# Kernel tuning notes

Hardware: AMD Instinct MI355X
Metric: run time of the kernel (lower is better)

## Reference

```python
import jax, jax.numpy as jnp
import numpy as np

B, S, D_IN, D_OUT = 4, 4096, 1024, 64

def setup_inputs() -> dict:
    key = jax.random.key(0)
    ks = jax.random.split(key, 7)
    return {
        "x":  jax.random.normal(ks[0], (B, S, D_IN), dtype=jnp.float32),
        "Wq": jax.random.normal(ks[1], (D_IN, D_OUT), dtype=jnp.float32) * 0.02,
        "bq": jax.random.normal(ks[2], (D_OUT,), dtype=jnp.float32) * 0.02,
        "Wk": jax.random.normal(ks[3], (D_IN, D_OUT), dtype=jnp.float32) * 0.02,
        "bk": jax.random.normal(ks[4], (D_OUT,), dtype=jnp.float32) * 0.02,
        "Wv": jax.random.normal(ks[5], (D_IN, D_OUT), dtype=jnp.float32) * 0.02,
        "bv": jax.random.normal(ks[6], (D_OUT,), dtype=jnp.float32) * 0.02,
    }

def reference(x, Wq, bq, Wk, bk, Wv, bv):
    # x: [B, S, d_in]
    seq = x.shape[1]
    q = x @ Wq + bq            # [B, S, d_out]
    k = x @ Wk + bk
    v = x @ Wv + bv
    scores = jnp.einsum("bqd,bkd->bqk", q, k)          # [B, S, S]
    causal = jnp.triu(jnp.ones((seq, seq), dtype=bool), k=1)
    scores = jnp.where(causal[None, :, :], -jnp.inf, scores)
    # NOTE: original code scales by sqrt(token_len), not sqrt(d_out) (d_k = keys.shape[1])
    scale = jnp.sqrt(jnp.asarray(seq, dtype=scores.dtype))
    attn = jax.nn.softmax(scores / scale, axis=-1)      # [B, S, S]
    # dropout in the original is applied but its result is discarded -> no-op
    return jnp.einsum("bqk,bkd->bqd", attn, v)          # [B, S, d_out]
```

## Files before the change

kernel.cpp:

```cpp
#include <hip/hip_runtime.h>
#include <math.h>

#define B 4
#define S 4096
#define DIN 1024
#define DOUT 64
#define BS (B * S)

typedef __bf16 bf16;
typedef __bf16 bf16x4 __attribute__((ext_vector_type(4)));
typedef __bf16 bf16x8 __attribute__((ext_vector_type(8)));
typedef float f32x4 __attribute__((ext_vector_type(4)));

#define QSCALE 0.022542110013890053f

#define QS_OFF 0
#define KF_OFF (2u * 1024 * 1024)
#define VF_OFF (4u * 1024 * 1024)
#define WP_OFF (6u * 1024 * 1024)
#define OP_OFF (7u * 1024 * 1024)
#define LP_OFF (23u * 1024 * 1024)

__global__ __launch_bounds__(256) void wpack_kernel(
    const float* __restrict__ Wq, const float* __restrict__ Wk,
    const float* __restrict__ Wv, bf16* __restrict__ wp) {
  const int t = blockIdx.x * 256 + threadIdx.x;
  const int m = t >> 16;
  const int r = t & 65535;
  const int k = r >> 6;
  const int n64 = r & 63;
  const float* W = (m == 0) ? Wq : (m == 1) ? Wk : Wv;
  const float v = W[r];
  const int n = m * 64 + n64;
  const int nt = n >> 4;
  const int lane = ((k >> 3) & 3) * 16 + (n & 15);
  const int idx = ((nt * 32 + (k >> 5)) * 64 + lane) * 8 + (k & 7);
  wp[idx] = (bf16)v;
}

__global__ __launch_bounds__(256) void qkv_mfma_kernel(
    const float* __restrict__ x, const float* __restrict__ bq,
    const float* __restrict__ bk, const float* __restrict__ bv,
    const bf16* __restrict__ wp, bf16* __restrict__ Qs,
    bf16* __restrict__ KF, bf16* __restrict__ VF) {
  __shared__ __align__(16) bf16 xt[32][520];

  const int tid = threadIdx.x;
  const int wid = tid >> 6;
  const int lane = tid & 63;
  const int l15 = lane & 15;
  const int quad = lane >> 4;
  const int blk = blockIdx.x;

  const bf16x8* wp8 = (const bf16x8*)wp;

  f32x4 acc[3][2];
#pragma unroll
  for (int j = 0; j < 3; ++j)
#pragma unroll
    for (int st = 0; st < 2; ++st) acc[j][st] = (f32x4)(0.f);

  for (int ph = 0; ph < 2; ++ph) {
    if (ph) __syncthreads();
    {
      float4 v[16];
#pragma unroll
      for (int i = 0; i < 16; ++i) {
        const int ch = i * 256 + tid;
        const int row = ch >> 7;
        const int col4 = ch & 127;
        v[i] = *(const float4*)(x + (size_t)(blk * 32 + row) * DIN + ph * 512 +
                                col4 * 4);
      }
#pragma unroll
      for (int i = 0; i < 16; ++i) {
        const int ch = i * 256 + tid;
        const int row = ch >> 7;
        const int col4 = ch & 127;
        bf16x4 c;
        c[0] = (bf16)v[i].x; c[1] = (bf16)v[i].y;
        c[2] = (bf16)v[i].z; c[3] = (bf16)v[i].w;
        *(bf16x4*)&xt[row][col4 * 4] = c;
      }
    }
    __syncthreads();

#pragma unroll 4
    for (int kc = 0; kc < 16; ++kc) {
      bf16x8 bfr[3];
#pragma unroll
      for (int j = 0; j < 3; ++j)
        bfr[j] = wp8[((wid * 3 + j) * 32 + ph * 16 + kc) * 64 + lane];
      const bf16x8 a0 = *(const bf16x8*)&xt[l15][quad * 8 + kc * 32];
      const bf16x8 a1 = *(const bf16x8*)&xt[16 + l15][quad * 8 + kc * 32];
#pragma unroll
      for (int j = 0; j < 3; ++j) {
        acc[j][0] = __builtin_amdgcn_mfma_f32_16x16x32_bf16(a0, bfr[j], acc[j][0], 0, 0, 0);
        acc[j][1] = __builtin_amdgcn_mfma_f32_16x16x32_bf16(a1, bfr[j], acc[j][1], 0, 0, 0);
      }
    }
  }

#pragma unroll
  for (int j = 0; j < 3; ++j) {
    const int nt = wid * 3 + j;
    const int sel = nt >> 2;
    const int c = (nt & 3) * 16 + l15;
    const float bias = ((sel == 0) ? bq : (sel == 1) ? bk : bv)[c];
#pragma unroll
    for (int st = 0; st < 2; ++st) {
      const int row0 = blk * 32 + st * 16 + quad * 4;
      if (sel == 0) {
#pragma unroll
        for (int r = 0; r < 4; ++r)
          Qs[(size_t)(row0 + r) * DOUT + c] =
              (bf16)((acc[j][st][r] + bias) * QSCALE);
      } else if (sel == 1) {
        const size_t kb =
            ((size_t)(((row0 >> 6) * 4 + ((row0 >> 4) & 3)) * 2 + (c >> 5)) * 64 +
             ((c >> 3) & 3) * 16 + quad * 4) * 8 + (c & 7);
#pragma unroll
        for (int r = 0; r < 4; ++r)
          KF[kb + r * 8] = (bf16)(acc[j][st][r] + bias);
      } else {
        const size_t vb =
            ((size_t)(((row0 >> 6) * 2 + ((row0 >> 5) & 1)) * 4 + (c >> 4)) * 64 +
             (c & 15) + 16 * ((row0 >> 3) & 3)) * 8 + (row0 & 7);
        bf16x4 vv;
#pragma unroll
        for (int r = 0; r < 4; ++r) vv[r] = (bf16)(acc[j][st][r] + bias);
        *(bf16x4*)(VF + vb) = vv;
      }
    }
  }
}

__global__ __launch_bounds__(256) void attn_mfma_kernel(
    const bf16* __restrict__ Qs, const bf16* __restrict__ KFp,
    const bf16* __restrict__ VFp, bf16* __restrict__ Oh,
    float* __restrict__ lh) {
  __shared__ __align__(16) bf16 pw[4][32][72];

  const int tid = threadIdx.x;
  const int wid = tid >> 6;
  const int lane = tid & 63;
  const int l15 = lane & 15;
  const int quad = lane >> 4;
  const int b = blockIdx.x & 3;
  const int half = (blockIdx.x >> 2) & 1;
  const int s32 = 127 - (blockIdx.x >> 3);
  const int ntiles = (s32 >> 1) + 1;
  const int e = half * 4 + wid;
  const int t0 = (e * ntiles) >> 3;
  const int t1 = ((e + 1) * ntiles) >> 3;

  const bf16x8* KF8 = (const bf16x8*)KFp;
  const bf16x8* VF8 = (const bf16x8*)VFp;
  const int tb0 = b * 64;

  const bf16* Qb = Qs + ((size_t)b * S + s32 * 32) * DOUT;
  bf16x8 qf[2][2];
#pragma unroll
  for (int st = 0; st < 2; ++st)
#pragma unroll
    for (int k = 0; k < 2; ++k)
      qf[st][k] =
          *(const bf16x8*)(Qb + (st * 16 + l15) * DOUT + k * 32 + quad * 8);

  f32x4 o[2][4];
#pragma unroll
  for (int st = 0; st < 2; ++st)
#pragma unroll
    for (int i = 0; i < 4; ++i) o[st][i] = (f32x4)(0.f);
  f32x4 lsum[2] = {(f32x4)(0.f), (f32x4)(0.f)};

  for (int t = t0; t < t1; ++t) {
    const int tb = tb0 + t;
    bf16x8 kf[8], vf[8];
#pragma unroll
    for (int nt = 0; nt < 4; ++nt)
#pragma unroll
      for (int c = 0; c < 2; ++c)
        kf[nt * 2 + c] = KF8[(size_t)((tb * 4 + nt) * 2 + c) * 64 + lane];
#pragma unroll
    for (int c = 0; c < 2; ++c)
#pragma unroll
      for (int ntd = 0; ntd < 4; ++ntd)
        vf[c * 4 + ntd] = VF8[(size_t)((tb * 2 + c) * 4 + ntd) * 64 + lane];

    f32x4 s[2][4];
#pragma unroll
    for (int st = 0; st < 2; ++st)
#pragma unroll
      for (int nt = 0; nt < 4; ++nt) {
        s[st][nt] = __builtin_amdgcn_mfma_f32_16x16x32_bf16(
            qf[st][0], kf[nt * 2 + 0], (f32x4)(0.f), 0, 0, 0);
        s[st][nt] = __builtin_amdgcn_mfma_f32_16x16x32_bf16(
            qf[st][1], kf[nt * 2 + 1], s[st][nt], 0, 0, 0);
      }

    if (t == ntiles - 1) {
#pragma unroll
      for (int st = 0; st < 2; ++st)
#pragma unroll
        for (int nt = 0; nt < 4; ++nt) {
          const int key = t * 64 + nt * 16 + l15;
#pragma unroll
          for (int r = 0; r < 4; ++r) {
            const int qrow = s32 * 32 + st * 16 + quad * 4 + r;
            const float p = (key <= qrow) ? exp2f(fminf(s[st][nt][r], 44.f)) : 0.f;
            lsum[st][r] += p;
            pw[wid][st * 16 + quad * 4 + r][nt * 16 + l15] = (bf16)p;
          }
        }
    } else {
#pragma unroll
      for (int st = 0; st < 2; ++st)
#pragma unroll
        for (int nt = 0; nt < 4; ++nt)
#pragma unroll
          for (int r = 0; r < 4; ++r) {
            const float p = exp2f(fminf(s[st][nt][r], 44.f));
            lsum[st][r] += p;
            pw[wid][st * 16 + quad * 4 + r][nt * 16 + l15] = (bf16)p;
          }
    }

#pragma unroll
    for (int st = 0; st < 2; ++st) {
      const bf16x8 pf0 = *(const bf16x8*)&pw[wid][st * 16 + l15][quad * 8];
      const bf16x8 pf1 = *(const bf16x8*)&pw[wid][st * 16 + l15][32 + quad * 8];
#pragma unroll
      for (int ntd = 0; ntd < 4; ++ntd) {
        o[st][ntd] = __builtin_amdgcn_mfma_f32_16x16x32_bf16(
            pf0, vf[0 * 4 + ntd], o[st][ntd], 0, 0, 0);
        o[st][ntd] = __builtin_amdgcn_mfma_f32_16x16x32_bf16(
            pf1, vf[1 * 4 + ntd], o[st][ntd], 0, 0, 0);
      }
    }
  }

#pragma unroll
  for (int m = 1; m < 16; m <<= 1)
#pragma unroll
    for (int st = 0; st < 2; ++st)
#pragma unroll
      for (int r = 0; r < 4; ++r) lsum[st][r] += __shfl_xor(lsum[st][r], m, 64);

  const int slot = (b * 128 + s32) * 8 + e;
  if (l15 == 0) {
#pragma unroll
    for (int st = 0; st < 2; ++st)
#pragma unroll
      for (int r = 0; r < 4; ++r)
        lh[slot * 32 + st * 16 + quad * 4 + r] = lsum[st][r];
  }
#pragma unroll
  for (int st = 0; st < 2; ++st)
#pragma unroll
    for (int ntd = 0; ntd < 4; ++ntd)
#pragma unroll
      for (int r = 0; r < 4; ++r)
        Oh[(size_t)slot * 2048 + (st * 16 + quad * 4 + r) * 64 + ntd * 16 + l15] =
            (bf16)o[st][ntd][r];
}

__global__ __launch_bounds__(256) void combine_kernel(
    const bf16* __restrict__ Oh, const float* __restrict__ lh,
    float* __restrict__ out) {
  const int gid = blockIdx.x * 256 + threadIdx.x;
  const int token = gid >> 4;
  const int d4 = (gid & 15) * 4;
  const int b = token >> 12;
  const int s = token & 4095;
  const int s32 = s >> 5;
  const int qq = s & 31;
  const int slot0 = (b * 128 + s32) * 8;
  f32x4 acc = (f32x4)(0.f);
  float l = 0.f;
#pragma unroll
  for (int q = 0; q < 8; ++q) {
    const bf16x4 ov =
        *(const bf16x4*)(Oh + (size_t)(slot0 + q) * 2048 + qq * 64 + d4);
#pragma unroll
    for (int i = 0; i < 4; ++i) acc[i] += (float)ov[i];
    l += lh[(slot0 + q) * 32 + qq];
  }
  ((f32x4*)out)[gid] = acc * (1.f / l);
}

extern "C" void kernel_launch(void* const* d_in, const int* in_sizes, int n_in,
                              void* d_out, int out_size, void* d_ws,
                              size_t ws_size, hipStream_t stream) {
  const float* x  = (const float*)d_in[0];
  const float* Wq = (const float*)d_in[1];
  const float* bq = (const float*)d_in[2];
  const float* Wk = (const float*)d_in[3];
  const float* bk = (const float*)d_in[4];
  const float* Wv = (const float*)d_in[5];
  const float* bv = (const float*)d_in[6];
  float* out = (float*)d_out;

  char* ws = (char*)d_ws;
  bf16* Qs = (bf16*)(ws + QS_OFF);
  bf16* KF = (bf16*)(ws + KF_OFF);
  bf16* VF = (bf16*)(ws + VF_OFF);
  bf16* wp = (bf16*)(ws + WP_OFF);
  bf16* Oh = (bf16*)(ws + OP_OFF);
  float* lh = (float*)(ws + LP_OFF);

  wpack_kernel<<<768, 256, 0, stream>>>(Wq, Wk, Wv, wp);
  qkv_mfma_kernel<<<512, 256, 0, stream>>>(x, bq, bk, bv, wp, Qs, KF, VF);
  attn_mfma_kernel<<<1024, 256, 0, stream>>>(Qs, KF, VF, Oh, lh);
  combine_kernel<<<1024, 256, 0, stream>>>(Oh, lh, out);
}
```

Before: 148.1 us.

## Split QKV projection across Q/K/V blocks with double-buffered x tiles; prefetch K in attention

The QKV kernel now launches three blocks per 32-row tile, one each for Q, K and V. Each block streams x in 128-column chunks through a double-buffered shared tile so the next global load overlaps the MFMA work, and shared memory per block drops, which should raise occupancy. The cost is that x is read three times from global memory. In the attention kernel, K fragments for the next tile are prefetched, and the causal mask is merged into a single branch-free path via a klim offset. Launch bounds are raised to hint at more resident waves.

```diff
diff --git a/kernel.cpp b/kernel.cpp
--- a/kernel.cpp
+++ b/kernel.cpp
@@ -38,104 +38,103 @@
   wp[idx] = (bf16)v;
 }
 
-__global__ __launch_bounds__(256) void qkv_mfma_kernel(
+__global__ __launch_bounds__(256, 6) void qkv_mfma_kernel(
     const float* __restrict__ x, const float* __restrict__ bq,
     const float* __restrict__ bk, const float* __restrict__ bv,
     const bf16* __restrict__ wp, bf16* __restrict__ Qs,
     bf16* __restrict__ KF, bf16* __restrict__ VF) {
-  __shared__ __align__(16) bf16 xt[32][520];
+  __shared__ __align__(16) bf16 xt[2][32][136];
 
   const int tid = threadIdx.x;
   const int wid = tid >> 6;
   const int lane = tid & 63;
   const int l15 = lane & 15;
   const int quad = lane >> 4;
-  const int blk = blockIdx.x;
-
+  const int sel = blockIdx.x % 3;
+  const int blk = blockIdx.x / 3;
+  const int nt = sel * 4 + wid;
+
+  const int srow = tid >> 3;
+  const int sc4 = tid & 7;
+  const float* xrow = x + (size_t)(blk * 32 + srow) * DIN + sc4 * 4;
   const bf16x8* wp8 = (const bf16x8*)wp;
 
-  f32x4 acc[3][2];
-#pragma unroll
-  for (int j = 0; j < 3; ++j)
-#pragma unroll
-    for (int st = 0; st < 2; ++st) acc[j][st] = (f32x4)(0.f);
-
-  for (int ph = 0; ph < 2; ++ph) {
-    if (ph) __syncthreads();
-    {
-      float4 v[16];
-#pragma unroll
-      for (int i = 0; i < 16; ++i) {
-        const int ch = i * 256 + tid;
-        const int row = ch >> 7;
-        const int col4 = ch & 127;
-        v[i] = *(const float4*)(x + (size_t)(blk * 32 + row) * DIN + ph * 512 +
-                                col4 * 4);
+  f32x4 acc[2] = {(f32x4)(0.f), (f32x4)(0.f)};
+
+  {
+    float4 pf[4];
+#pragma unroll
+    for (int i = 0; i < 4; ++i) pf[i] = *(const float4*)(xrow + i * 32);
+#pragma unroll
+    for (int i = 0; i < 4; ++i) {
+      bf16x4 c;
+      c[0] = (bf16)pf[i].x; c[1] = (bf16)pf[i].y;
+      c[2] = (bf16)pf[i].z; c[3] = (bf16)pf[i].w;
+      *(bf16x4*)&xt[0][srow][i * 32 + sc4 * 4] = c;
+    }
+  }
+  __syncthreads();
+
+  for (int p = 0; p < 8; ++p) {
+    const int buf = p & 1;
+    float4 pf[4];
+    if (p < 7) {
+#pragma unroll
+      for (int i = 0; i < 4; ++i)
+        pf[i] = *(const float4*)(xrow + (p + 1) * 128 + i * 32);
+    }
+#pragma unroll
+    for (int i = 0; i < 4; ++i) {
+      const int kc = p * 4 + i;
+      const bf16x8 bfr = wp8[(nt * 32 + kc) * 64 + lane];
+      const bf16x8 a0 = *(const bf16x8*)&xt[buf][l15][i * 32 + quad * 8];
+      const bf16x8 a1 = *(const bf16x8*)&xt[buf][16 + l15][i * 32 + quad * 8];
+      acc[0] = __builtin_amdgcn_mfma_f32_16x16x32_bf16(a0, bfr, acc[0], 0, 0, 0);
+      acc[1] = __builtin_amdgcn_mfma_f32_16x16x32_bf16(a1, bfr, acc[1], 0, 0, 0);
+    }
+    if (p < 7) {
+      __syncthreads();
+#pragma unroll
+      for (int i = 0; i < 4; ++i) {
+        bf16x4 c;
+        c[0] = (bf16)pf[i].x; c[1] = (bf16)pf[i].y;
+        c[2] = (bf16)pf[i].z; c[3] = (bf16)pf[i].w;
+        *(bf16x4*)&xt[buf ^ 1][srow][i * 32 + sc4 * 4] = c;
       }
-#pragma unroll
-      for (int i = 0; i < 16; ++i) {
-        const int ch = i * 256 + tid;
-        const int row = ch >> 7;
-        const int col4 = ch & 127;
-        bf16x4 c;
-        c[0] = (bf16)v[i].x; c[1] = (bf16)v[i].y;
-        c[2] = (bf16)v[i].z; c[3] = (bf16)v[i].w;
-        *(bf16x4*)&xt[row][col4 * 4] = c;
-      }
-    }
-    __syncthreads();
-
-#pragma unroll 4
-    for (int kc = 0; kc < 16; ++kc) {
-      bf16x8 bfr[3];
-#pragma unroll
-      for (int j = 0; j < 3; ++j)
-        bfr[j] = wp8[((wid * 3 + j) * 32 + ph * 16 + kc) * 64 + lane];
-      const bf16x8 a0 = *(const bf16x8*)&xt[l15][quad * 8 + kc * 32];
-      const bf16x8 a1 = *(const bf16x8*)&xt[16 + l15][quad * 8 + kc * 32];
-#pragma unroll
-      for (int j = 0; j < 3; ++j) {
-        acc[j][0] = __builtin_amdgcn_mfma_f32_16x16x32_bf16(a0, bfr[j], acc[j][0], 0, 0, 0);
-        acc[j][1] = __builtin_amdgcn_mfma_f32_16x16x32_bf16(a1, bfr[j], acc[j][1], 0, 0, 0);
-      }
-    }
-  }
-
-#pragma unroll
-  for (int j = 0; j < 3; ++j) {
-    const int nt = wid * 3 + j;
-    const int sel = nt >> 2;
-    const int c = (nt & 3) * 16 + l15;
-    const float bias = ((sel == 0) ? bq : (sel == 1) ? bk : bv)[c];
-#pragma unroll
-    for (int st = 0; st < 2; ++st) {
-      const int row0 = blk * 32 + st * 16 + quad * 4;
-      if (sel == 0) {
-#pragma unroll
-        for (int r = 0; r < 4; ++r)
-          Qs[(size_t)(row0 + r) * DOUT + c] =
-              (bf16)((acc[j][st][r] + bias) * QSCALE);
-      } else if (sel == 1) {
-        const size_t kb =
-            ((size_t)(((row0 >> 6) * 4 + ((row0 >> 4) & 3)) * 2 + (c >> 5)) * 64 +
-             ((c >> 3) & 3) * 16 + quad * 4) * 8 + (c & 7);
-#pragma unroll
-        for (int r = 0; r < 4; ++r)
-          KF[kb + r * 8] = (bf16)(acc[j][st][r] + bias);
-      } else {
-        const size_t vb =
-            ((size_t)(((row0 >> 6) * 2 + ((row0 >> 5) & 1)) * 4 + (c >> 4)) * 64 +
-             (c & 15) + 16 * ((row0 >> 3) & 3)) * 8 + (row0 & 7);
-        bf16x4 vv;
-#pragma unroll
-        for (int r = 0; r < 4; ++r) vv[r] = (bf16)(acc[j][st][r] + bias);
-        *(bf16x4*)(VF + vb) = vv;
-      }
-    }
-  }
-}
-
-__global__ __launch_bounds__(256) void attn_mfma_kernel(
+      __syncthreads();
+    }
+  }
+
+  const int c = wid * 16 + l15;
+  const float bias = ((sel == 0) ? bq : (sel == 1) ? bk : bv)[c];
+#pragma unroll
+  for (int st = 0; st < 2; ++st) {
+    const int row0 = blk * 32 + st * 16 + quad * 4;
+    if (sel == 0) {
+#pragma unroll
+      for (int r = 0; r < 4; ++r)
+        Qs[(size_t)(row0 + r) * DOUT + c] =
+            (bf16)((acc[st][r] + bias) * QSCALE);
+    } else if (sel == 1) {
+      const size_t kb =
+          ((size_t)(((row0 >> 6) * 4 + ((row0 >> 4) & 3)) * 2 + (c >> 5)) * 64 +
+           ((c >> 3) & 3) * 16 + quad * 4) * 8 + (c & 7);
+#pragma unroll
+      for (int r = 0; r < 4; ++r)
+        KF[kb + r * 8] = (bf16)(acc[st][r] + bias);
+    } else {
+      const size_t vb =
+          ((size_t)(((row0 >> 6) * 2 + ((row0 >> 5) & 1)) * 4 + (c >> 4)) * 64 +
+           (c & 15) + 16 * ((row0 >> 3) & 3)) * 8 + (row0 & 7);
+      bf16x4 vv;
+#pragma unroll
+      for (int r = 0; r < 4; ++r) vv[r] = (bf16)(acc[st][r] + bias);
+      *(bf16x4*)(VF + vb) = vv;
+    }
+  }
+}
+
+__global__ __launch_bounds__(256, 3) void attn_mfma_kernel(
     const bf16* __restrict__ Qs, const bf16* __restrict__ KFp,
     const bf16* __restrict__ VFp, bf16* __restrict__ Oh,
     float* __restrict__ lh) {
@@ -174,56 +173,56 @@
     for (int i = 0; i < 4; ++i) o[st][i] = (f32x4)(0.f);
   f32x4 lsum[2] = {(f32x4)(0.f), (f32x4)(0.f)};
 
+  bf16x8 kf[8];
+  if (t0 < t1) {
+    const int tb = tb0 + t0;
+#pragma unroll
+    for (int nt = 0; nt < 4; ++nt)
+#pragma unroll
+      for (int c = 0; c < 2; ++c)
+        kf[nt * 2 + c] = KF8[(size_t)((tb * 4 + nt) * 2 + c) * 64 + lane];
+  }
+
   for (int t = t0; t < t1; ++t) {
     const int tb = tb0 + t;
-    bf16x8 kf[8], vf[8];
-#pragma unroll
-    for (int nt = 0; nt < 4; ++nt)
-#pragma unroll
-      for (int c = 0; c < 2; ++c)
-        kf[nt * 2 + c] = KF8[(size_t)((tb * 4 + nt) * 2 + c) * 64 + lane];
+    bf16x8 vf[8];
 #pragma unroll
     for (int c = 0; c < 2; ++c)
 #pragma unroll
       for (int ntd = 0; ntd < 4; ++ntd)
         vf[c * 4 + ntd] = VF8[(size_t)((tb * 2 + c) * 4 + ntd) * 64 + lane];
 
-    f32x4 s[2][4];
-#pragma unroll
-    for (int st = 0; st < 2; ++st)
-#pragma unroll
-      for (int nt = 0; nt < 4; ++nt) {
-        s[st][nt] = __builtin_amdgcn_mfma_f32_16x16x32_bf16(
-            qf[st][0], kf[nt * 2 + 0], (f32x4)(0.f), 0, 0, 0);
-        s[st][nt] = __builtin_amdgcn_mfma_f32_16x16x32_bf16(
-            qf[st][1], kf[nt * 2 + 1], s[st][nt], 0, 0, 0);
+    const int klim = (t == ntiles - 1) ? 0 : (1 << 24);
+#pragma unroll
+    for (int nt = 0; nt < 4; ++nt) {
+      f32x4 s0 = __builtin_amdgcn_mfma_f32_16x16x32_bf16(
+          qf[0][0], kf[nt * 2 + 0], (f32x4)(0.f), 0, 0, 0);
+      s0 = __builtin_amdgcn_mfma_f32_16x16x32_bf16(qf[0][1], kf[nt * 2 + 1],
+                                                   s0, 0, 0, 0);
+      f32x4 s1 = __builtin_amdgcn_mfma_f32_16x16x32_bf16(
+          qf[1][0], kf[nt * 2 + 0], (f32x4)(0.f), 0, 0, 0);
+      s1 = __builtin_amdgcn_mfma_f32_16x16x32_bf16(qf[1][1], kf[nt * 2 + 1],
+                                                   s1, 0, 0, 0);
+      const int key = t * 64 + nt * 16 + l15;
+#pragma unroll
+      for (int r = 0; r < 4; ++r) {
+        const int q0 = s32 * 32 + quad * 4 + r + klim;
+        const float p0 = (key <= q0) ? exp2f(fminf(s0[r], 44.f)) : 0.f;
+        lsum[0][r] += p0;
+        pw[wid][quad * 4 + r][nt * 16 + l15] = (bf16)p0;
+        const float p1 = (key <= q0 + 16) ? exp2f(fminf(s1[r], 44.f)) : 0.f;
+        lsum[1][r] += p1;
+        pw[wid][16 + quad * 4 + r][nt * 16 + l15] = (bf16)p1;
       }
-
-    if (t == ntiles - 1) {
-#pragma unroll
-      for (int st = 0; st < 2; ++st)
-#pragma unroll
-        for (int nt = 0; nt < 4; ++nt) {
-          const int key = t * 64 + nt * 16 + l15;
-#pragma unroll
-          for (int r = 0; r < 4; ++r) {
-            const int qrow = s32 * 32 + st * 16 + quad * 4 + r;
-            const float p = (key <= qrow) ? exp2f(fminf(s[st][nt][r], 44.f)) : 0.f;
-            lsum[st][r] += p;
-            pw[wid][st * 16 + quad * 4 + r][nt * 16 + l15] = (bf16)p;
-          }
-        }
-    } else {
-#pragma unroll
-      for (int st = 0; st < 2; ++st)
-#pragma unroll
-        for (int nt = 0; nt < 4; ++nt)
-#pragma unroll
-          for (int r = 0; r < 4; ++r) {
-            const float p = exp2f(fminf(s[st][nt][r], 44.f));
-            lsum[st][r] += p;
-            pw[wid][st * 16 + quad * 4 + r][nt * 16 + l15] = (bf16)p;
-          }
+    }
+
+    if (t + 1 < t1) {
+      const int tbn = tb + 1;
+#pragma unroll
+      for (int nt = 0; nt < 4; ++nt)
+#pragma unroll
+        for (int c = 0; c < 2; ++c)
+          kf[nt * 2 + c] = KF8[(size_t)((tbn * 4 + nt) * 2 + c) * 64 + lane];
     }
 
 #pragma unroll
@@ -310,7 +309,7 @@
   float* lh = (float*)(ws + LP_OFF);
 
   wpack_kernel<<<768, 256, 0, stream>>>(Wq, Wk, Wv, wp);
-  qkv_mfma_kernel<<<512, 256, 0, stream>>>(x, bq, bk, bv, wp, Qs, KF, VF);
+  qkv_mfma_kernel<<<1536, 256, 0, stream>>>(x, bq, bk, bv, wp, Qs, KF, VF);
   attn_mfma_kernel<<<1024, 256, 0, stream>>>(Qs, KF, VF, Oh, lh);
   combine_kernel<<<1024, 256, 0, stream>>>(Oh, lh, out);
 }
```

Result: slower. 155.3 us (+4.8%).
